# Kernel optimization log

Measured on AMD Instinct MI355X. Metric: run time of the kernel, lower is better.

Reference implementation:

```python
import jax, jax.numpy as jnp
import numpy as np

K_KNN = 20
TC = 3  # taylor_channel
N_TERMS = 20  # trivariate polynomial terms up to order 3
CHANNELS = [(6, 32), (32, 64), (64, 128), (128, 256)]


def _knn_indices(xyz, k):
    sq = jnp.sum(xyz * xyz, axis=1)  # B x N
    d2 = sq[:, :, None] + sq[:, None, :] - 2.0 * jnp.einsum('bci,bcj->bij', xyz, xyz)
    _, idx = jax.lax.top_k(-d2, k)
    return idx


def _group(feat, idx):
    # feat: B x C x N, idx: B x N x K -> B x C x N x K
    return jax.vmap(lambda f, i: f[:, i])(feat, idx)


def _taylor_terms(g):
    X, Y, Z = g[:, 0], g[:, 1], g[:, 2]
    one = jnp.ones_like(X)
    terms = [one, X, Y, Z, X * Y, X * Z, Y * Z, X * X, Y * Y, Z * Z,
             X * X * Y, X * X * Z, X * Y * Y, Y * Y * Z, X * Z * Z, Y * Z * Z,
             X * Y * Z, X * X * X, Y * Y * Y, Z * Z * Z]
    return jnp.stack(terms, axis=1)


def _spider_conv(feat, idx, terms, w1, b1, w2, b2):
    # feat: B x C x N; w1: tc x 20; w2: out x (C*tc) x K
    B, C, N = feat.shape
    g = _group(feat, idx)  # B x C x N x K
    taylor = jnp.einsum('btnk,ot->bonk', terms, w1) + b1[None, :, None, None]
    g = (g[:, :, None, :, :] * taylor[:, None, :, :, :]).reshape(B, C * TC, N, g.shape[-1])
    out = jnp.einsum('bcnk,ock->bon', g, w2) + b2[None, :, None]
    return jax.nn.relu(out)


def _forward(pc, params):
    # pc: B x N x 6
    pcT = jnp.transpose(pc, (0, 2, 1))
    xyz = pcT[:, 0:3, :]
    idx = _knn_indices(xyz, K_KNN)  # B x N x K
    grouped_xyz = _group(xyz, idx)
    grouped_pc = grouped_xyz - xyz[:, :, :, None]  # relative coords
    terms = _taylor_terms(grouped_pc)
    feat = pcT
    feats = []
    for l in range(4):
        w1, b1, w2, b2 = params[l]
        feat = _spider_conv(feat, idx, terms, w1, b1, w2, b2)
        feats.append(feat)
    cat = jnp.concatenate(feats, axis=1)
    top2, _ = jax.lax.top_k(cat, 2)  # topk over point dim (last axis)
    return top2.reshape(cat.shape[0], -1)  # B x 960


def setup_inputs() -> dict:
    key = jax.random.key(0)
    keys = jax.random.split(key, 1 + 16)
    B, N = 4, 2048
    inp = {'pc': jax.random.normal(keys[0], (B, N, 6), dtype=jnp.float32)}
    ki = 1
    for l, (cin, cout) in enumerate(CHANNELS):
        inp[f'w1_{l}'] = jax.random.normal(keys[ki], (TC, N_TERMS), dtype=jnp.float32) * 0.1; ki += 1
        inp[f'b1_{l}'] = jax.random.normal(keys[ki], (TC,), dtype=jnp.float32) * 0.01; ki += 1
        inp[f'w2_{l}'] = jax.random.normal(keys[ki], (cout, cin * TC, K_KNN), dtype=jnp.float32) * (1.0 / np.sqrt(cin * TC * K_KNN)); ki += 1
        inp[f'b2_{l}'] = jax.random.normal(keys[ki], (cout,), dtype=jnp.float32) * 0.01; ki += 1
    return inp


def reference(pc, w1_0, b1_0, w2_0, b2_0, w1_1, b1_1, w2_1, b2_1,
              w1_2, b1_2, w2_2, b2_2, w1_3, b1_3, w2_3, b2_3):
    params = [(w1_0, b1_0, w2_0, b2_0), (w1_1, b1_1, w2_1, b2_1),
              (w1_2, b1_2, w2_2, b2_2), (w1_3, b1_3, w2_3, b2_3)]
    return _forward(pc, params)
```

## Files before the change

kernel.cpp:

```cpp
#include <hip/hip_runtime.h>
#include <math.h>

#define BB 4
#define NN 2048
#define KNN 20

typedef _Float16 f16x8 __attribute__((ext_vector_type(8)));
typedef _Float16 f16x4 __attribute__((ext_vector_type(4)));
typedef _Float16 f16x2 __attribute__((ext_vector_type(2)));
typedef float f32x4 __attribute__((ext_vector_type(4)));

#define DPP_STEP(CTRL, RMASK)                                                   \
    {                                                                           \
        unsigned ov = (unsigned)__builtin_amdgcn_update_dpp(                    \
            (int)bv, (int)bv, CTRL, RMASK, 0xf, false);                         \
        unsigned oj = (unsigned)__builtin_amdgcn_update_dpp(                    \
            (int)jj, (int)jj, CTRL, RMASK, 0xf, false);                         \
        bool lt = (ov < bv) || (ov == bv && oj < jj);                           \
        bv = lt ? ov : bv;                                                      \
        jj = lt ? oj : jj;                                                      \
    }

__global__ __launch_bounds__(256) void knn_kernel(const float* __restrict__ pc,
                                                  int* __restrict__ idx_out,
                                                  float* __restrict__ rel_out) {
    __shared__ float4 sp[NN];
    const int tid = threadIdx.x;
    const int b = blockIdx.x / (NN / 4);
    const int grp = blockIdx.x % (NN / 4);
    for (int p = tid; p < NN; p += 256) {
        float x = pc[(size_t)(b * NN + p) * 6 + 0];
        float y = pc[(size_t)(b * NN + p) * 6 + 1];
        float z = pc[(size_t)(b * NN + p) * 6 + 2];
        float4 v;
        v.x = x; v.y = y; v.z = z;
        v.w = __fadd_rn(__fadd_rn(__fmul_rn(x, x), __fmul_rn(y, y)), __fmul_rn(z, z));
        sp[p] = v;
    }
    __syncthreads();
    const int lane = tid & 63;
    const int i = grp * 4 + (tid >> 6);
    const float4 pi = sp[i];
    const float xi = pi.x, yi = pi.y, zi = pi.z, sqi = pi.w;

    unsigned mmr[32];
#pragma unroll
    for (int t = 0; t < 32; ++t) {
        const int j = t * 64 + lane;
        const float4 pj = sp[j];
        float dot = __fadd_rn(__fadd_rn(__fmul_rn(xi, pj.x), __fmul_rn(yi, pj.y)),
                              __fmul_rn(zi, pj.z));
        float d2 = __fsub_rn(__fadd_rn(sqi, pj.w), __fmul_rn(2.0f, dot));
        unsigned bbits = __float_as_uint(d2);
        mmr[t] = bbits ^ (0x80000000u | (unsigned)((int)bbits >> 31));
    }

    const unsigned UMAX = 0xFFFFFFFFu;
    unsigned mask = 0u;
    unsigned v1, t1, v2, t2;

    auto refill = [&]() {
        v1 = UMAX; t1 = 0u; v2 = UMAX; t2 = 0u;
#pragma unroll
        for (int t = 0; t < 32; ++t) {
            unsigned m = ((mask >> t) & 1u) ? UMAX : mmr[t];
            bool c1 = m < v1;
            bool c2 = m < v2;
            unsigned nv2 = c1 ? v1 : (c2 ? m : v2);
            unsigned nt2 = c1 ? t1 : (c2 ? (unsigned)t : t2);
            v1 = c1 ? m : v1;
            t1 = c1 ? (unsigned)t : t1;
            v2 = nv2; t2 = nt2;
        }
    };
    refill();

    const size_t orow = (size_t)(b * NN + i);
    for (int k = 0; k < KNN; ++k) {
        unsigned bv = v1;
        unsigned jj = (t1 << 6) | (unsigned)lane;
        DPP_STEP(0x111, 0xf)
        DPP_STEP(0x112, 0xf)
        DPP_STEP(0x114, 0xf)
        DPP_STEP(0x118, 0xf)
        DPP_STEP(0x142, 0xa)
        DPP_STEP(0x143, 0xc)
        const unsigned sj = (unsigned)__builtin_amdgcn_readlane((int)jj, 63);
        if (lane == 0) {
            idx_out[orow * KNN + k] = (int)sj;
            const float4 pj = sp[sj];
            size_t ro = (orow * KNN + k) * 3;
            rel_out[ro + 0] = __fsub_rn(pj.x, xi);
            rel_out[ro + 1] = __fsub_rn(pj.y, yi);
            rel_out[ro + 2] = __fsub_rn(pj.z, zi);
        }
        if (k < KNN - 1) {
            bool am = ((sj & 63u) == (unsigned)lane);
            if (am) {
                mask |= (1u << (sj >> 6));
                v1 = v2; t1 = t2; v2 = UMAX;
            }
            if (__ballot(v1 == UMAX) != 0ull) refill();
        }
    }
}

__global__ __launch_bounds__(256) void taylor_all_kernel(
    const float* __restrict__ rel,
    const float* __restrict__ w10, const float* __restrict__ b10, _Float16* __restrict__ ty0,
    const float* __restrict__ w11, const float* __restrict__ b11, _Float16* __restrict__ ty1,
    const float* __restrict__ w12, const float* __restrict__ b12, _Float16* __restrict__ ty2,
    const float* __restrict__ w13, const float* __restrict__ b13, _Float16* __restrict__ ty3) {
    __shared__ float w1s[4][60];
    __shared__ float b1s[4][3];
    const int tid = threadIdx.x;
    if (tid < 240) {
        const float* wp = (tid < 60) ? w10 : (tid < 120) ? w11 : (tid < 180) ? w12 : w13;
        w1s[tid / 60][tid % 60] = wp[tid % 60];
    } else if (tid < 252) {
        int r = tid - 240;
        const float* bp = (r < 3) ? b10 : (r < 6) ? b11 : (r < 9) ? b12 : b13;
        b1s[r / 3][r % 3] = bp[r % 3];
    }
    __syncthreads();
    int t = blockIdx.x * 256 + tid;
    if (t >= BB * NN * KNN) return;
    float X = rel[(size_t)t * 3 + 0], Y = rel[(size_t)t * 3 + 1], Z = rel[(size_t)t * 3 + 2];
    float tm[20];
    tm[0] = 1.f; tm[1] = X; tm[2] = Y; tm[3] = Z;
    tm[4] = X * Y; tm[5] = X * Z; tm[6] = Y * Z;
    tm[7] = X * X; tm[8] = Y * Y; tm[9] = Z * Z;
    tm[10] = X * X * Y; tm[11] = X * X * Z; tm[12] = X * Y * Y; tm[13] = Y * Y * Z;
    tm[14] = X * Z * Z; tm[15] = Y * Z * Z; tm[16] = X * Y * Z;
    tm[17] = X * X * X; tm[18] = Y * Y * Y; tm[19] = Z * Z * Z;
    _Float16* typ[4] = {ty0, ty1, ty2, ty3};
#pragma unroll
    for (int l = 0; l < 4; ++l) {
#pragma unroll
        for (int o = 0; o < 3; ++o) {
            float a = b1s[l][o];
#pragma unroll
            for (int q = 0; q < 20; ++q) a += w1s[l][o * 20 + q] * tm[q];
            typ[l][(size_t)t * 3 + o] = (_Float16)a;
        }
    }
}

struct WsplitArgs {
    const float* w2[4];
    _Float16* wf[4];
    int COUT[4], CIN[4], CPAD[4], OCB[4], KCB[4];
    int cum[4];
};

__global__ __launch_bounds__(256) void wsplit_all_kernel(WsplitArgs a) {
    int e = blockIdx.x * 256 + threadIdx.x;
    if (e >= a.cum[3]) return;
    int l = (e >= a.cum[0]) + (e >= a.cum[1]) + (e >= a.cum[2]);
    int base = l ? a.cum[l - 1] : 0;
    e -= base;
    const int KCB = a.KCB[l], OCB = a.OCB[l], CPAD = a.CPAD[l], CIN = a.CIN[l];
    int i = e & 7;
    int lane = (e >> 3) & 63;
    int fi = e >> 9;
    int kcb = fi % KCB;
    int ocb = (fi / KCB) % OCB;
    int k = fi / (KCB * OCB);
    int oc = ocb * 16 + (lane & 15);
    int kk = kcb * 32 + (lane >> 4) * 8 + i;
    int o = kk / CPAD, c = kk % CPAD;
    float x = 0.f;
    if (o < 3 && c < CIN)
        x = a.w2[l][((size_t)oc * (CIN * 3) + c * 3 + o) * KNN + k];
    a.wf[l][e] = (_Float16)x;
}

template <int CIN, int COUT, int CK3P, int NT, int WM, int WN, int FM, int FN,
          int OCT, int KSPLIT, bool L0S>
__global__ __launch_bounds__(256) void convm_kernel(const float* __restrict__ fin,
                                                    const int* __restrict__ idx,
                                                    const _Float16* __restrict__ tyg,
                                                    const _Float16* __restrict__ wf,
                                                    float* __restrict__ out) {
    constexpr int KR = KNN / KSPLIT;
    constexpr int SR = CK3P + 8;
    constexpr int KCB = CK3P / 32;
    constexpr int OCB = COUT / 16;
    constexpr int OCBLK = WM * FM * 16;
    constexpr int NTL = NN / NT;
    constexpr int TPR = 256 / NT;
    constexpr int CT = L0S ? 6 : (CIN / TPR);
    constexpr int CQ = L0S ? 2 : (CT / 4);
    static_assert(WN * FN * 16 == NT, "n tiling");
    static_assert(OCBLK * OCT == COUT, "oc tiling");
    static_assert(WM * WN == 4, "4 waves");

    __shared__ _Float16 Bs[NT * SR];
    __shared__ _Float16 tyt[NT][3 * KR];
    __shared__ int idxt[NT][KR];

    const int tid = threadIdx.x;
    const int lane = tid & 63;
    const int wid = tid >> 6;
    const int wm = wid / WN;
    const int wn = wid % WN;
    int t = blockIdx.x;
    const int b = t % BB;      t /= BB;
    const int ks = t % KSPLIT; t /= KSPLIT;
    const int oct = t % OCT;   t /= OCT;
    const int ntl = t;
    const int n0 = ntl * NT;
    const int oc0 = oct * OCBLK;
    const int k0 = ks * KR;
    const size_t brow = (size_t)b * NN;

    for (int e = tid; e < NT * KR; e += 256) {
        int n = e / KR, kk = e % KR;
        idxt[n][kk] = idx[(brow + n0 + n) * KNN + k0 + kk];
    }
    for (int e = tid; e < NT * 3 * KR; e += 256) {
        int n = e / (3 * KR), q = e % (3 * KR);
        tyt[n][q] = tyg[((brow + n0 + n) * KNN + k0) * 3 + q];
    }
    __syncthreads();

    const int nrow = tid % NT;
    const int sub = tid / NT;
    float4 g[CQ];

    auto issue_gather = [&](int kk) {
        if constexpr (L0S) {
            if (tid < 192) {
                int j = idxt[nrow][kk];
                const float* p = fin + (brow + j) * 6;
                g[0] = *reinterpret_cast<const float4*>(p);
                float2 r2 = *reinterpret_cast<const float2*>(p + 4);
                g[1].x = r2.x; g[1].y = r2.y;
            }
        } else {
            int j = idxt[nrow][kk];
            const float* p = fin + (brow + j) * CIN + sub * CT;
#pragma unroll
            for (int q = 0; q < CQ; ++q)
                g[q] = *reinterpret_cast<const float4*>(p + q * 4);
        }
    };
    issue_gather(0);

    f32x4 acc[FM][FN];
#pragma unroll
    for (int fm = 0; fm < FM; ++fm)
#pragma unroll
        for (int fn = 0; fn < FN; ++fn) acc[fm][fn] = (f32x4){0.f, 0.f, 0.f, 0.f};

    f16x8 areg[FM * KCB];
    auto loadA_burst = [&](int k) {
#pragma unroll
        for (int fm = 0; fm < FM; ++fm)
#pragma unroll
            for (int kcb = 0; kcb < KCB; ++kcb) {
                size_t fidx = ((size_t)k * OCB + (oc0 >> 4) + wm * FM + fm) * KCB + kcb;
                areg[fm * KCB + kcb] =
                    *reinterpret_cast<const f16x8*>(&wf[(fidx * 64 + lane) * 8]);
            }
    };

    for (int kk = 0; kk < KR; ++kk) {
        const int k = k0 + kk;
        loadA_burst(k);
        __syncthreads();
        if constexpr (L0S) {
            if (tid < 192) {
                _Float16 th = tyt[nrow][kk * 3 + sub];
                f16x2 tb; tb[0] = th; tb[1] = th;
                f16x2 g0, g1, g2;
                g0[0] = (_Float16)g[0].x; g0[1] = (_Float16)g[0].y;
                g1[0] = (_Float16)g[0].z; g1[1] = (_Float16)g[0].w;
                g2[0] = (_Float16)g[1].x; g2[1] = (_Float16)g[1].y;
                f16x2 p0 = g0 * tb, p1 = g1 * tb, p2 = g2 * tb;
                f16x8 hv;
                hv[0] = p0[0]; hv[1] = p0[1]; hv[2] = p1[0]; hv[3] = p1[1];
                hv[4] = p2[0]; hv[5] = p2[1]; hv[6] = (_Float16)0.f; hv[7] = (_Float16)0.f;
                *reinterpret_cast<f16x8*>(&Bs[nrow * SR + sub * 8]) = hv;
                if (sub == 0) {
                    f16x8 z = {};
                    *reinterpret_cast<f16x8*>(&Bs[nrow * SR + 24]) = z;
                }
            }
        } else {
            f16x2 gh[CT / 2];
#pragma unroll
            for (int q = 0; q < CQ; ++q) {
                f16x2 a0, a1;
                a0[0] = (_Float16)g[q].x; a0[1] = (_Float16)g[q].y;
                a1[0] = (_Float16)g[q].z; a1[1] = (_Float16)g[q].w;
                gh[2 * q] = a0; gh[2 * q + 1] = a1;
            }
            _Float16 th0 = tyt[nrow][kk * 3 + 0];
            _Float16 th1 = tyt[nrow][kk * 3 + 1];
            _Float16 th2 = tyt[nrow][kk * 3 + 2];
#pragma unroll
            for (int o = 0; o < 3; ++o) {
                _Float16 th = (o == 0) ? th0 : (o == 1) ? th1 : th2;
                f16x2 tb; tb[0] = th; tb[1] = th;
#pragma unroll
                for (int qp = 0; qp < CT / 8; ++qp) {
                    f16x2 p0 = gh[4 * qp + 0] * tb;
                    f16x2 p1 = gh[4 * qp + 1] * tb;
                    f16x2 p2 = gh[4 * qp + 2] * tb;
                    f16x2 p3 = gh[4 * qp + 3] * tb;
                    f16x8 hv;
                    hv[0] = p0[0]; hv[1] = p0[1]; hv[2] = p1[0]; hv[3] = p1[1];
                    hv[4] = p2[0]; hv[5] = p2[1]; hv[6] = p3[0]; hv[7] = p3[1];
                    *reinterpret_cast<f16x8*>(
                        &Bs[nrow * SR + o * CIN + sub * CT + qp * 8]) = hv;
                }
            }
        }
        __syncthreads();
        if (kk + 1 < KR) issue_gather(kk + 1);
#pragma unroll
        for (int kcb = 0; kcb < KCB; ++kcb) {
            f16x8 bf[FN];
#pragma unroll
            for (int fn = 0; fn < FN; ++fn) {
                int row = wn * FN * 16 + fn * 16 + (lane & 15);
                bf[fn] = *reinterpret_cast<const f16x8*>(
                    &Bs[row * SR + kcb * 32 + (lane >> 4) * 8]);
            }
#pragma unroll
            for (int fm = 0; fm < FM; ++fm)
#pragma unroll
                for (int fn = 0; fn < FN; ++fn)
                    acc[fm][fn] = __builtin_amdgcn_mfma_f32_16x16x32_f16(
                        areg[fm * KCB + kcb], bf[fn], acc[fm][fn], 0, 0, 0);
        }
    }
    float* dst = out + (size_t)ks * ((size_t)BB * NN * COUT);
#pragma unroll
    for (int fm = 0; fm < FM; ++fm) {
        const int ocb = oc0 + wm * FM * 16 + fm * 16 + ((lane >> 4) << 2);
#pragma unroll
        for (int fn = 0; fn < FN; ++fn) {
            int n = n0 + wn * FN * 16 + fn * 16 + (lane & 15);
            float4 o4;
            o4.x = acc[fm][fn][0]; o4.y = acc[fm][fn][1];
            o4.z = acc[fm][fn][2]; o4.w = acc[fm][fn][3];
            *reinterpret_cast<float4*>(&dst[(brow + n) * COUT + ocb]) = o4;
        }
    }
}

template <int CIN, int COUT, int CK3P, int NT, int WM, int WN, int FM, int FN,
          int OCT, int KSPLIT>
__global__ __launch_bounds__(256) void convp_kernel(const float* __restrict__ fin,
                                                    const int* __restrict__ idx,
                                                    const _Float16* __restrict__ tyg,
                                                    const _Float16* __restrict__ wf,
                                                    float* __restrict__ out) {
    constexpr int KR = KNN / KSPLIT;
    constexpr int SR = CK3P + 8;
    constexpr int CKH = CK3P / 2;
    constexpr int KCB = CK3P / 32;
    constexpr int KCBH = KCB / 2;
    constexpr int OCB = COUT / 16;
    constexpr int OCBLK = WM * FM * 16;
    constexpr int NTL = NN / NT;
    constexpr int TPR = 256 / NT;
    constexpr int CT = CIN / TPR;
    constexpr int CQ = CT / 4;
    static_assert(WN * FN * 16 == NT, "n tiling");
    static_assert(OCBLK * OCT == COUT, "oc tiling");
    static_assert(WM * WN == 4, "4 waves");

    __shared__ _Float16 Bs[NT * SR];
    __shared__ _Float16 tyt[NT][3 * KR];
    __shared__ int idxt[NT][KR];

    const int tid = threadIdx.x;
    const int lane = tid & 63;
    const int wid = tid >> 6;
    const int wm = wid / WN;
    const int wn = wid % WN;
    int t = blockIdx.x;
    const int b = t % BB;      t /= BB;
    const int ks = t % KSPLIT; t /= KSPLIT;
    const int oct = t % OCT;   t /= OCT;
    const int ntl = t;
    const int n0 = ntl * NT;
    const int oc0 = oct * OCBLK;
    const int k0 = ks * KR;
    const size_t brow = (size_t)b * NN;

    for (int e = tid; e < NT * KR; e += 256) {
        int n = e / KR, kk = e % KR;
        idxt[n][kk] = idx[(brow + n0 + n) * KNN + k0 + kk];
    }
    for (int e = tid; e < NT * 3 * KR; e += 256) {
        int n = e / (3 * KR), q = e % (3 * KR);
        tyt[n][q] = tyg[((brow + n0 + n) * KNN + k0) * 3 + q];
    }
    __syncthreads();

    const int nrow = tid % NT;
    const int sub = tid / NT;
    float4 g[CQ];
    f16x2 gh[CT / 2];

    auto issue_gather = [&](int kk) {
        int j = idxt[nrow][kk];
        const float* p = fin + (brow + j) * CIN + sub * CT;
#pragma unroll
        for (int q = 0; q < CQ; ++q)
            g[q] = *reinterpret_cast<const float4*>(p + q * 4);
    };
    auto convert_gh = [&]() {
#pragma unroll
        for (int q = 0; q < CQ; ++q) {
            f16x2 a0, a1;
            a0[0] = (_Float16)g[q].x; a0[1] = (_Float16)g[q].y;
            a1[0] = (_Float16)g[q].z; a1[1] = (_Float16)g[q].w;
            gh[2 * q] = a0; gh[2 * q + 1] = a1;
        }
    };
    auto buildB = [&](int h, int kk) {
        _Float16 th0 = tyt[nrow][kk * 3 + 0];
        _Float16 th1 = tyt[nrow][kk * 3 + 1];
        _Float16 th2 = tyt[nrow][kk * 3 + 2];
#pragma unroll
        for (int o = 0; o < 3; ++o) {
            const int kkpos = o * CIN + sub * CT;
            if (kkpos / CKH != h) continue;
            _Float16 th = (o == 0) ? th0 : (o == 1) ? th1 : th2;
            f16x2 tb; tb[0] = th; tb[1] = th;
#pragma unroll
            for (int qp = 0; qp < CT / 8; ++qp) {
                f16x2 p0 = gh[4 * qp + 0] * tb;
                f16x2 p1 = gh[4 * qp + 1] * tb;
                f16x2 p2 = gh[4 * qp + 2] * tb;
                f16x2 p3 = gh[4 * qp + 3] * tb;
                f16x8 hv;
                hv[0] = p0[0]; hv[1] = p0[1]; hv[2] = p1[0]; hv[3] = p1[1];
                hv[4] = p2[0]; hv[5] = p2[1]; hv[6] = p3[0]; hv[7] = p3[1];
                *reinterpret_cast<f16x8*>(&Bs[nrow * SR + kkpos + qp * 8]) = hv;
            }
        }
    };

    f32x4 acc[FM][FN];
#pragma unroll
    for (int fm = 0; fm < FM; ++fm)
#pragma unroll
        for (int fn = 0; fn < FN; ++fn) acc[fm][fn] = (f32x4){0.f, 0.f, 0.f, 0.f};

    f16x8 regA[FM * KCBH], regB[FM * KCBH];
    auto loadA = [&](int k, int h, f16x8* dst) {
#pragma unroll
        for (int fm = 0; fm < FM; ++fm)
#pragma unroll
            for (int kcb = 0; kcb < KCBH; ++kcb) {
                size_t fidx = ((size_t)k * OCB + (oc0 >> 4) + wm * FM + fm) * KCB +
                              h * KCBH + kcb;
                dst[fm * KCBH + kcb] =
                    *reinterpret_cast<const f16x8*>(&wf[(fidx * 64 + lane) * 8]);
            }
    };
    auto mfma_half = [&](int h, const f16x8* areg) {
#pragma unroll
        for (int kcb = 0; kcb < KCBH; ++kcb) {
            const int kabs = h * KCBH + kcb;
            f16x8 bf[FN];
#pragma unroll
            for (int fn = 0; fn < FN; ++fn) {
                int row = wn * FN * 16 + fn * 16 + (lane & 15);
                bf[fn] = *reinterpret_cast<const f16x8*>(
                    &Bs[row * SR + kabs * 32 + (lane >> 4) * 8]);
            }
#pragma unroll
            for (int fm = 0; fm < FM; ++fm)
#pragma unroll
                for (int fn = 0; fn < FN; ++fn)
                    acc[fm][fn] = __builtin_amdgcn_mfma_f32_16x16x32_f16(
                        areg[fm * KCBH + kcb], bf[fn], acc[fm][fn], 0, 0, 0);
        }
    };

    issue_gather(0);
    convert_gh();
    loadA(k0, 0, regA);
    buildB(0, 0);
    __syncthreads();

    for (int kk = 0; kk < KR; ++kk) {
        const int k = k0 + kk;
        loadA(k, 1, regB);
        if (kk + 1 < KR) issue_gather(kk + 1);
        buildB(1, kk);
        mfma_half(0, regA);
        __syncthreads();
        if (kk + 1 < KR) {
            loadA(k + 1, 0, regA);
            convert_gh();
            buildB(0, kk + 1);
        }
        mfma_half(1, regB);
        __syncthreads();
    }

    float* dst = out + (size_t)ks * ((size_t)BB * NN * COUT);
#pragma unroll
    for (int fm = 0; fm < FM; ++fm) {
        const int ocb = oc0 + wm * FM * 16 + fm * 16 + ((lane >> 4) << 2);
#pragma unroll
        for (int fn = 0; fn < FN; ++fn) {
            int n = n0 + wn * FN * 16 + fn * 16 + (lane & 15);
            float4 o4;
            o4.x = acc[fm][fn][0]; o4.y = acc[fm][fn][1];
            o4.z = acc[fm][fn][2]; o4.w = acc[fm][fn][3];
            *reinterpret_cast<float4*>(&dst[(brow + n) * COUT + ocb]) = o4;
        }
    }
}

template <int COUT, int KS>
__global__ __launch_bounds__(256) void combine_kernel(const float* __restrict__ p,
                                                      const float* __restrict__ b2,
                                                      float* __restrict__ out) {
    constexpr size_t TOT = (size_t)BB * NN * COUT;
    size_t i = (size_t)blockIdx.x * 256 + threadIdx.x;
    if (i * 4 >= TOT) return;
    const float4* p4 = reinterpret_cast<const float4*>(p);
    float4 a = p4[i];
#pragma unroll
    for (int s = 1; s < KS; ++s) {
        float4 v = p4[i + s * (TOT / 4)];
        a.x += v.x; a.y += v.y; a.z += v.z; a.w += v.w;
    }
    float4 bb = *reinterpret_cast<const float4*>(&b2[(i * 4) % COUT]);
    float4 r;
    r.x = fmaxf(a.x + bb.x, 0.f); r.y = fmaxf(a.y + bb.y, 0.f);
    r.z = fmaxf(a.z + bb.z, 0.f); r.w = fmaxf(a.w + bb.w, 0.f);
    reinterpret_cast<float4*>(out)[i] = r;
}

__global__ __launch_bounds__(256) void top2_kernel(const float* __restrict__ f1,
                                                   const float* __restrict__ f2,
                                                   const float* __restrict__ f3,
                                                   const float* __restrict__ p3,
                                                   const float* __restrict__ b23,
                                                   float* __restrict__ out) {
    __shared__ float m1s[256], m2s[256];
    const int bid = blockIdx.x;
    const int b = bid / 480;
    const int ch = bid % 480;
    const size_t brow = (size_t)b * NN;
    float m1 = -INFINITY, m2 = -INFINITY;
    if (ch < 224) {
        const float* f; int C, c;
        if (ch < 32)       { f = f1; C = 32;  c = ch; }
        else if (ch < 96)  { f = f2; C = 64;  c = ch - 32; }
        else               { f = f3; C = 128; c = ch - 96; }
        for (int n = threadIdx.x; n < NN; n += 256) {
            float v = f[(brow + n) * C + c];
            if (v > m1) { m2 = m1; m1 = v; }
            else if (v > m2) m2 = v;
        }
    } else {
        const int c = ch - 224;
        const float bc = b23[c];
        constexpr size_t TOT3 = (size_t)BB * NN * 256;
        for (int n = threadIdx.x; n < NN; n += 256) {
            size_t o = (brow + n) * 256 + c;
            float v = fmaxf(p3[o] + p3[TOT3 + o] + bc, 0.f);
            if (v > m1) { m2 = m1; m1 = v; }
            else if (v > m2) m2 = v;
        }
    }
    m1s[threadIdx.x] = m1; m2s[threadIdx.x] = m2;
    __syncthreads();
    for (int s = 128; s > 0; s >>= 1) {
        if (threadIdx.x < s) {
            float a1 = m1s[threadIdx.x], a2 = m2s[threadIdx.x];
            float c1 = m1s[threadIdx.x + s], c2 = m2s[threadIdx.x + s];
            m1s[threadIdx.x] = fmaxf(a1, c1);
            m2s[threadIdx.x] = fmaxf(fminf(a1, c1), fmaxf(a2, c2));
        }
        __syncthreads();
    }
    if (threadIdx.x == 0) {
        out[(size_t)b * 960 + ch * 2 + 0] = m1s[0];
        out[(size_t)b * 960 + ch * 2 + 1] = m2s[0];
    }
}

extern "C" void kernel_launch(void* const* d_in, const int* in_sizes, int n_in,
                              void* d_out, int out_size, void* d_ws, size_t ws_size,
                              hipStream_t stream) {
    const float* pc = (const float*)d_in[0];
    const float *w1[4], *b1[4], *w2[4], *b2[4];
    for (int l = 0; l < 4; ++l) {
        w1[l] = (const float*)d_in[1 + 4 * l];
        b1[l] = (const float*)d_in[2 + 4 * l];
        w2[l] = (const float*)d_in[3 + 4 * l];
        b2[l] = (const float*)d_in[4 + 4 * l];
    }
    char* ws = (char*)d_ws;
    size_t off = 0;
    auto alloc = [&](size_t bytes) -> void* {
        void* p = ws + off;
        off = (off + bytes + 255) & ~(size_t)255;
        return p;
    };
    int* idxb      = (int*)alloc((size_t)BB * NN * KNN * 4);
    float* rel     = (float*)alloc((size_t)BB * NN * KNN * 3 * 4);
    _Float16* ty0  = (_Float16*)alloc((size_t)BB * NN * KNN * 3 * 2);
    _Float16* ty1  = (_Float16*)alloc((size_t)BB * NN * KNN * 3 * 2);
    _Float16* ty2  = (_Float16*)alloc((size_t)BB * NN * KNN * 3 * 2);
    _Float16* ty3  = (_Float16*)alloc((size_t)BB * NN * KNN * 3 * 2);
    const int wtot0 = KNN * 2 * 1 * 512;
    const int wtot1 = KNN * 4 * 3 * 512;
    const int wtot2 = KNN * 8 * 6 * 512;
    const int wtot3 = KNN * 16 * 12 * 512;
    _Float16* wf0 = (_Float16*)alloc((size_t)wtot0 * 2);
    _Float16* wf1 = (_Float16*)alloc((size_t)wtot1 * 2);
    _Float16* wf2 = (_Float16*)alloc((size_t)wtot2 * 2);
    _Float16* wf3 = (_Float16*)alloc((size_t)wtot3 * 2);
    float* f1     = (float*)alloc((size_t)BB * NN * 32 * 4);
    float* f2     = (float*)alloc((size_t)BB * NN * 64 * 4);
    float* f3     = (float*)alloc((size_t)BB * NN * 128 * 4);
    float* pbuf   = (float*)alloc((size_t)4 * BB * NN * 128 * 4);

    knn_kernel<<<BB * NN / 4, 256, 0, stream>>>(pc, idxb, rel);

    taylor_all_kernel<<<(BB * NN * KNN + 255) / 256, 256, 0, stream>>>(
        rel, w1[0], b1[0], ty0, w1[1], b1[1], ty1, w1[2], b1[2], ty2, w1[3], b1[3], ty3);

    WsplitArgs wa;
    wa.w2[0] = w2[0]; wa.w2[1] = w2[1]; wa.w2[2] = w2[2]; wa.w2[3] = w2[3];
    wa.wf[0] = wf0; wa.wf[1] = wf1; wa.wf[2] = wf2; wa.wf[3] = wf3;
    int COUTs[4] = {32, 64, 128, 256}, CINs[4] = {6, 32, 64, 128};
    int CPADs[4] = {8, 32, 64, 128}, OCBs[4] = {2, 4, 8, 16}, KCBs[4] = {1, 3, 6, 12};
    int cum = 0;
    for (int l = 0; l < 4; ++l) {
        wa.COUT[l] = COUTs[l]; wa.CIN[l] = CINs[l]; wa.CPAD[l] = CPADs[l];
        wa.OCB[l] = OCBs[l]; wa.KCB[l] = KCBs[l];
        cum += KNN * OCBs[l] * KCBs[l] * 512;
        wa.cum[l] = cum;
    }
    wsplit_all_kernel<<<(cum + 255) / 256, 256, 0, stream>>>(wa);

    convm_kernel<6, 32, 32, 64, 2, 2, 1, 2, 1, 4, true>
        <<<512, 256, 0, stream>>>(pc, idxb, ty0, wf0, pbuf);
    combine_kernel<32, 4><<<(BB * NN * 32 / 4 + 255) / 256, 256, 0, stream>>>(pbuf, b2[0], f1);

    convm_kernel<32, 64, 96, 64, 4, 1, 1, 4, 1, 4, false>
        <<<512, 256, 0, stream>>>(f1, idxb, ty1, wf1, pbuf);
    combine_kernel<64, 4><<<(BB * NN * 64 / 4 + 255) / 256, 256, 0, stream>>>(pbuf, b2[1], f2);

    convm_kernel<64, 128, 192, 64, 4, 1, 2, 4, 1, 4, false>
        <<<512, 256, 0, stream>>>(f2, idxb, ty2, wf2, pbuf);
    combine_kernel<128, 4><<<(BB * NN * 128 / 4 + 255) / 256, 256, 0, stream>>>(pbuf, b2[2], f3);

    convp_kernel<128, 256, 384, 64, 4, 1, 2, 4, 2, 2>
        <<<512, 256, 0, stream>>>(f3, idxb, ty3, wf3, pbuf);

    top2_kernel<<<BB * 480, 256, 0, stream>>>(f1, f2, f3, pbuf, b2[3], (float*)d_out);
}
```

Baseline: 187.1 us.

## Store intermediate layer features in fp16 and gather half-precision inputs

The combine kernel now writes layer outputs f1–f3 as fp16 instead of fp32. The conv kernels gather f16x8 vectors directly, skipping the fp32 load and conversion, and top2 reads the fp16 buffers. Layer 2 also switches from the convm kernel to the pipelined convp kernel. This halves gather bandwidth and intermediate storage, at the cost of rounding the stored activations, and therefore the top-2 outputs for layers 0–2, to fp16.

```diff
diff --git a/kernel.cpp b/kernel.cpp
--- a/kernel.cpp
+++ b/kernel.cpp
@@ -176,8 +176,8 @@
 }
 
 template <int CIN, int COUT, int CK3P, int NT, int WM, int WN, int FM, int FN,
-          int OCT, int KSPLIT, bool L0S>
-__global__ __launch_bounds__(256) void convm_kernel(const float* __restrict__ fin,
+          int OCT, int KSPLIT, bool L0S, bool F16IN>
+__global__ __launch_bounds__(256) void convm_kernel(const void* __restrict__ fin,
                                                     const int* __restrict__ idx,
                                                     const _Float16* __restrict__ tyg,
                                                     const _Float16* __restrict__ wf,
@@ -190,7 +190,8 @@
     constexpr int NTL = NN / NT;
     constexpr int TPR = 256 / NT;
     constexpr int CT = L0S ? 6 : (CIN / TPR);
-    constexpr int CQ = L0S ? 2 : (CT / 4);
+    constexpr int CQ = L0S ? 2 : (CT >= 4 ? CT / 4 : 1);
+    constexpr int GF = (CT >= 8) ? CT / 8 : 1;
     static_assert(WN * FN * 16 == NT, "n tiling");
     static_assert(OCBLK * OCT == COUT, "oc tiling");
     static_assert(WM * WN == 4, "4 waves");
@@ -198,6 +199,9 @@
     __shared__ _Float16 Bs[NT * SR];
     __shared__ _Float16 tyt[NT][3 * KR];
     __shared__ int idxt[NT][KR];
+
+    const float* finf = (const float*)fin;
+    const _Float16* finh = (const _Float16*)fin;
 
     const int tid = threadIdx.x;
     const int lane = tid & 63;
@@ -227,19 +231,26 @@
     const int nrow = tid % NT;
     const int sub = tid / NT;
     float4 g[CQ];
+    f16x8 gf[GF];
 
     auto issue_gather = [&](int kk) {
         if constexpr (L0S) {
             if (tid < 192) {
                 int j = idxt[nrow][kk];
-                const float* p = fin + (brow + j) * 6;
+                const float* p = finf + (brow + j) * 6;
                 g[0] = *reinterpret_cast<const float4*>(p);
                 float2 r2 = *reinterpret_cast<const float2*>(p + 4);
                 g[1].x = r2.x; g[1].y = r2.y;
             }
+        } else if constexpr (F16IN) {
+            int j = idxt[nrow][kk];
+            const _Float16* p = finh + (brow + j) * CIN + sub * CT;
+#pragma unroll
+            for (int q = 0; q < GF; ++q)
+                gf[q] = *reinterpret_cast<const f16x8*>(p + q * 8);
         } else {
             int j = idxt[nrow][kk];
-            const float* p = fin + (brow + j) * CIN + sub * CT;
+            const float* p = finf + (brow + j) * CIN + sub * CT;
 #pragma unroll
             for (int q = 0; q < CQ; ++q)
                 g[q] = *reinterpret_cast<const float4*>(p + q * 4);
@@ -289,12 +300,18 @@
             }
         } else {
             f16x2 gh[CT / 2];
-#pragma unroll
-            for (int q = 0; q < CQ; ++q) {
-                f16x2 a0, a1;
-                a0[0] = (_Float16)g[q].x; a0[1] = (_Float16)g[q].y;
-                a1[0] = (_Float16)g[q].z; a1[1] = (_Float16)g[q].w;
-                gh[2 * q] = a0; gh[2 * q + 1] = a1;
+            if constexpr (F16IN) {
+                const f16x2* gp = reinterpret_cast<const f16x2*>(gf);
+#pragma unroll
+                for (int q = 0; q < CT / 2; ++q) gh[q] = gp[q];
+            } else {
+#pragma unroll
+                for (int q = 0; q < CQ; ++q) {
+                    f16x2 a0, a1;
+                    a0[0] = (_Float16)g[q].x; a0[1] = (_Float16)g[q].y;
+                    a1[0] = (_Float16)g[q].z; a1[1] = (_Float16)g[q].w;
+                    gh[2 * q] = a0; gh[2 * q + 1] = a1;
+                }
             }
             _Float16 th0 = tyt[nrow][kk * 3 + 0];
             _Float16 th1 = tyt[nrow][kk * 3 + 1];
@@ -353,7 +370,7 @@
 
 template <int CIN, int COUT, int CK3P, int NT, int WM, int WN, int FM, int FN,
           int OCT, int KSPLIT>
-__global__ __launch_bounds__(256) void convp_kernel(const float* __restrict__ fin,
+__global__ __launch_bounds__(256) void convp_kernel(const _Float16* __restrict__ fin,
                                                     const int* __restrict__ idx,
                                                     const _Float16* __restrict__ tyg,
                                                     const _Float16* __restrict__ wf,
@@ -368,7 +385,7 @@
     constexpr int NTL = NN / NT;
     constexpr int TPR = 256 / NT;
     constexpr int CT = CIN / TPR;
-    constexpr int CQ = CT / 4;
+    constexpr int GF = CT / 8;
     static_assert(WN * FN * 16 == NT, "n tiling");
     static_assert(OCBLK * OCT == COUT, "oc tiling");
     static_assert(WM * WN == 4, "4 waves");
@@ -404,24 +421,20 @@
 
     const int nrow = tid % NT;
     const int sub = tid / NT;
-    float4 g[CQ];
-    f16x2 gh[CT / 2];
+    f16x8 gnext[GF];
+    f16x2 ghc[CT / 2];
 
     auto issue_gather = [&](int kk) {
         int j = idxt[nrow][kk];
-        const float* p = fin + (brow + j) * CIN + sub * CT;
-#pragma unroll
-        for (int q = 0; q < CQ; ++q)
-            g[q] = *reinterpret_cast<const float4*>(p + q * 4);
-    };
-    auto convert_gh = [&]() {
-#pragma unroll
-        for (int q = 0; q < CQ; ++q) {
-            f16x2 a0, a1;
-            a0[0] = (_Float16)g[q].x; a0[1] = (_Float16)g[q].y;
-            a1[0] = (_Float16)g[q].z; a1[1] = (_Float16)g[q].w;
-            gh[2 * q] = a0; gh[2 * q + 1] = a1;
-        }
+        const _Float16* p = fin + (brow + j) * CIN + sub * CT;
+#pragma unroll
+        for (int q = 0; q < GF; ++q)
+            gnext[q] = *reinterpret_cast<const f16x8*>(p + q * 8);
+    };
+    auto commit_gh = [&]() {
+        const f16x2* gp = reinterpret_cast<const f16x2*>(gnext);
+#pragma unroll
+        for (int q = 0; q < CT / 2; ++q) ghc[q] = gp[q];
     };
     auto buildB = [&](int h, int kk) {
         _Float16 th0 = tyt[nrow][kk * 3 + 0];
@@ -435,10 +448,10 @@
             f16x2 tb; tb[0] = th; tb[1] = th;
 #pragma unroll
             for (int qp = 0; qp < CT / 8; ++qp) {
-                f16x2 p0 = gh[4 * qp + 0] * tb;
-                f16x2 p1 = gh[4 * qp + 1] * tb;
-                f16x2 p2 = gh[4 * qp + 2] * tb;
-                f16x2 p3 = gh[4 * qp + 3] * tb;
+                f16x2 p0 = ghc[4 * qp + 0] * tb;
+                f16x2 p1 = ghc[4 * qp + 1] * tb;
+                f16x2 p2 = ghc[4 * qp + 2] * tb;
+                f16x2 p3 = ghc[4 * qp + 3] * tb;
                 f16x8 hv;
                 hv[0] = p0[0]; hv[1] = p0[1]; hv[2] = p1[0]; hv[3] = p1[1];
                 hv[4] = p2[0]; hv[5] = p2[1]; hv[6] = p3[0]; hv[7] = p3[1];
@@ -486,7 +499,7 @@
     };
 
     issue_gather(0);
-    convert_gh();
+    commit_gh();
     loadA(k0, 0, regA);
     buildB(0, 0);
     __syncthreads();
@@ -500,7 +513,7 @@
         __syncthreads();
         if (kk + 1 < KR) {
             loadA(k + 1, 0, regA);
-            convert_gh();
+            commit_gh();
             buildB(0, kk + 1);
         }
         mfma_half(1, regB);
@@ -525,7 +538,7 @@
 template <int COUT, int KS>
 __global__ __launch_bounds__(256) void combine_kernel(const float* __restrict__ p,
                                                       const float* __restrict__ b2,
-                                                      float* __restrict__ out) {
+                                                      _Float16* __restrict__ out) {
     constexpr size_t TOT = (size_t)BB * NN * COUT;
     size_t i = (size_t)blockIdx.x * 256 + threadIdx.x;
     if (i * 4 >= TOT) return;
@@ -537,15 +550,17 @@
         a.x += v.x; a.y += v.y; a.z += v.z; a.w += v.w;
     }
     float4 bb = *reinterpret_cast<const float4*>(&b2[(i * 4) % COUT]);
-    float4 r;
-    r.x = fmaxf(a.x + bb.x, 0.f); r.y = fmaxf(a.y + bb.y, 0.f);
-    r.z = fmaxf(a.z + bb.z, 0.f); r.w = fmaxf(a.w + bb.w, 0.f);
-    reinterpret_cast<float4*>(out)[i] = r;
-}
-
-__global__ __launch_bounds__(256) void top2_kernel(const float* __restrict__ f1,
-                                                   const float* __restrict__ f2,
-                                                   const float* __restrict__ f3,
+    f16x4 r;
+    r[0] = (_Float16)fmaxf(a.x + bb.x, 0.f);
+    r[1] = (_Float16)fmaxf(a.y + bb.y, 0.f);
+    r[2] = (_Float16)fmaxf(a.z + bb.z, 0.f);
+    r[3] = (_Float16)fmaxf(a.w + bb.w, 0.f);
+    *reinterpret_cast<f16x4*>(&out[i * 4]) = r;
+}
+
+__global__ __launch_bounds__(256) void top2_kernel(const _Float16* __restrict__ f1,
+                                                   const _Float16* __restrict__ f2,
+                                                   const _Float16* __restrict__ f3,
                                                    const float* __restrict__ p3,
                                                    const float* __restrict__ b23,
                                                    float* __restrict__ out) {
@@ -556,12 +571,12 @@
     const size_t brow = (size_t)b * NN;
     float m1 = -INFINITY, m2 = -INFINITY;
     if (ch < 224) {
-        const float* f; int C, c;
+        const _Float16* f; int C, c;
         if (ch < 32)       { f = f1; C = 32;  c = ch; }
         else if (ch < 96)  { f = f2; C = 64;  c = ch - 32; }
         else               { f = f3; C = 128; c = ch - 96; }
         for (int n = threadIdx.x; n < NN; n += 256) {
-            float v = f[(brow + n) * C + c];
+            float v = (float)f[(brow + n) * C + c];
             if (v > m1) { m2 = m1; m1 = v; }
             else if (v > m2) m2 = v;
         }
@@ -625,9 +640,9 @@
     _Float16* wf1 = (_Float16*)alloc((size_t)wtot1 * 2);
     _Float16* wf2 = (_Float16*)alloc((size_t)wtot2 * 2);
     _Float16* wf3 = (_Float16*)alloc((size_t)wtot3 * 2);
-    float* f1     = (float*)alloc((size_t)BB * NN * 32 * 4);
-    float* f2     = (float*)alloc((size_t)BB * NN * 64 * 4);
-    float* f3     = (float*)alloc((size_t)BB * NN * 128 * 4);
+    _Float16* f1  = (_Float16*)alloc((size_t)BB * NN * 32 * 2);
+    _Float16* f2  = (_Float16*)alloc((size_t)BB * NN * 64 * 2);
+    _Float16* f3  = (_Float16*)alloc((size_t)BB * NN * 128 * 2);
     float* pbuf   = (float*)alloc((size_t)4 * BB * NN * 128 * 4);
 
     knn_kernel<<<BB * NN / 4, 256, 0, stream>>>(pc, idxb, rel);
@@ -649,15 +664,15 @@
     }
     wsplit_all_kernel<<<(cum + 255) / 256, 256, 0, stream>>>(wa);
 
-    convm_kernel<6, 32, 32, 64, 2, 2, 1, 2, 1, 4, true>
+    convm_kernel<6, 32, 32, 64, 2, 2, 1, 2, 1, 4, true, false>
         <<<512, 256, 0, stream>>>(pc, idxb, ty0, wf0, pbuf);
     combine_kernel<32, 4><<<(BB * NN * 32 / 4 + 255) / 256, 256, 0, stream>>>(pbuf, b2[0], f1);
 
-    convm_kernel<32, 64, 96, 64, 4, 1, 1, 4, 1, 4, false>
+    convm_kernel<32, 64, 96, 64, 4, 1, 1, 4, 1, 4, false, true>
         <<<512, 256, 0, stream>>>(f1, idxb, ty1, wf1, pbuf);
     combine_kernel<64, 4><<<(BB * NN * 64 / 4 + 255) / 256, 256, 0, stream>>>(pbuf, b2[1], f2);
 
-    convm_kernel<64, 128, 192, 64, 4, 1, 2, 4, 1, 4, false>
+    convp_kernel<64, 128, 192, 64, 4, 1, 2, 4, 1, 4>
         <<<512, 256, 0, stream>>>(f2, idxb, ty2, wf2, pbuf);
     combine_kernel<128, 4><<<(BB * NN * 128 / 4 + 255) / 256, 256, 0, stream>>>(pbuf, b2[2], f3);
 
```

Result: faster. 174.8 us (-6.6%).
